# Optimization experiments

Hardware: AMD Instinct MI355X
Metric: run time of the kernel (lower is better)

## Reference

```python
import jax, jax.numpy as jnp
import numpy as np

B, C, H, W = 4, 64, 64, 64  # x shape; mask is (B,1,8H,8W)


def _conv(x, w, pad=0):
    return jax.lax.conv_general_dilated(
        x, w, (1, 1), [(pad, pad), (pad, pad)],
        dimension_numbers=('NCHW', 'OIHW', 'NCHW'))


def _inorm(x, eps=1e-5):  # InstanceNorm2d, affine=False, biased var (torch default)
    mu = x.mean(axis=(2, 3), keepdims=True)
    var = x.var(axis=(2, 3), keepdims=True)
    return (x - mu) * jax.lax.rsqrt(var + eps)


def _forward(x, mask, kconv_w1, kconv_w2, fs_w1, fs_w2, fs_b2, fs_fuse_w):
    b, c, h, w = x.shape
    n = h * w
    # MaxPool2d(8,8) then binarize
    m = jax.lax.reduce_window(mask, -jnp.inf, jax.lax.max,
                              (1, 1, 8, 8), (1, 1, 8, 8), 'VALID')
    m = (m > 0).astype(x.dtype)
    back = 1.0 - m
    # ResidualBlock K_conv (shared for K and Q paths in original code)
    y = jax.nn.relu(_inorm(_conv(x, kconv_w1, pad=1)))
    y = _inorm(_conv(y, kconv_w2, pad=1))
    kx = jax.nn.relu(y + x)
    # L2-normalized K/Q over channel dim
    K = (kx * back).reshape(b, c, n)
    K = K / (jnp.linalg.norm(K, axis=1, keepdims=True) + 1e-8)
    Q = (kx * m).reshape(b, c, n)
    Q = Q / (jnp.linalg.norm(Q, axis=1, keepdims=True) + 1e-8)
    V = (x * back).reshape(b, c, n)
    # cosine-similarity score map, temperature 20
    score = jnp.einsum('bcq,bck->bqk', Q, K) * 20.0  # (b, n_q, n_k)
    qm = m.reshape(b, 1, n)      # query mask (foreground)
    km = back.reshape(b, 1, n)   # key mask (background)
    NEG = -1000000.0
    validx = score + (1.0 - km) * NEG + (1.0 - qm.transpose(0, 2, 1)) * NEG
    att = jax.nn.softmax(validx, axis=-1) * (qm.transpose(0, 2, 1) * km)
    # att_fore[b,c,q] = sum_k V[b,c,k] * att[b,q,k]
    att_fore = jnp.einsum('bck,bqk->bcq', V, att).reshape(b, c, h, w)
    # Fusion_score
    feat1 = _conv(jnp.concatenate([x * m, att_fore * m], axis=1), fs_w1)
    s = jax.nn.sigmoid(_conv(feat1, fs_w2) + fs_b2[None, :, None, None])
    fused = _conv(jnp.concatenate([x * m, att_fore * m * (1.0 - s)], axis=1), fs_fuse_w)
    fs_out = fused * m + x * (1.0 - m)
    out = fs_out * m + x * (1.0 - m)
    # visualization attention mask
    visatt = att.sum(axis=1).reshape(b, 1, h, w)
    attmask = jnp.repeat(jnp.repeat(visatt, 8, axis=2), 8, axis=3)  # nearest upsample x8
    attmask = attmask / attmask.max()
    return out, attmask


def setup_inputs() -> dict:
    key = jax.random.key(0)
    ks = jax.random.split(key, 8)

    def wgt(k, shape, fan_in):
        return jax.random.normal(k, shape, jnp.float32) / np.sqrt(fan_in)

    x = jax.random.normal(ks[0], (B, C, H, W), jnp.float32)
    # sparse foreground mask so maxpool(8x8)>0 yields a mixed fg/bg mask
    mask = (jax.random.uniform(ks[1], (B, 1, H * 8, W * 8)) < 0.01).astype(jnp.float32)
    return dict(
        x=x, mask=mask,
        kconv_w1=wgt(ks[2], (C, C, 3, 3), C * 9),
        kconv_w2=wgt(ks[3], (C, C, 3, 3), C * 9),
        fs_w1=wgt(ks[4], (C, 2 * C, 1, 1), 2 * C),
        fs_w2=wgt(ks[5], (C, C, 1, 1), C),
        fs_b2=jnp.zeros((C,), jnp.float32),
        fs_fuse_w=wgt(ks[6], (C, 2 * C, 1, 1), 2 * C),
    )


def reference(x, mask, kconv_w1, kconv_w2, fs_w1, fs_w2, fs_b2, fs_fuse_w):
    return _forward(x, mask, kconv_w1, kconv_w2, fs_w1, fs_w2, fs_b2, fs_fuse_w)
```

## Files before the change

kernel.cpp:

```cpp
#include <hip/hip_runtime.h>
#include <hip/hip_bf16.h>

typedef __hip_bfloat16 bf16;
typedef __attribute__((ext_vector_type(8))) short short8;
typedef __attribute__((ext_vector_type(4))) float f32x4;
typedef __attribute__((ext_vector_type(16))) float f32x16;

#define BB 4
#define CC 64
#define NN 4096
#define MH 512
#define MW 512
#define LS 72

#define WB_AFC  ((size_t)0)
#define WB_DEN  ((size_t)4194304)
#define WB_VIS  ((size_t)4259840)
#define WB_QIX  ((size_t)4325376)
#define WB_KIX  ((size_t)4390912)
#define WB_MFL  ((size_t)4456448)
#define WB_CNT  ((size_t)4472832)
#define WB_STAT ((size_t)4472896)
#define WB_WT1  ((size_t)4476992)
#define WB_WT2  ((size_t)4550720)
#define WB_WFB  ((size_t)4624448)

__device__ __forceinline__ float b2f(bf16 v) { return __bfloat162float(v); }
__device__ __forceinline__ float us2f(unsigned short u) { return __uint_as_float(((unsigned)u) << 16); }
__device__ __forceinline__ unsigned short f2bu(float f) {
  bf16 h = __float2bfloat16(f);
  return *(unsigned short*)&h;
}

__global__ __launch_bounds__(256) void k_maxpool(const float* __restrict__ mask,
                                                 unsigned char* __restrict__ mfl,
                                                 float* __restrict__ vis,
                                                 float* __restrict__ gstat,
                                                 unsigned int* __restrict__ vmaxb) {
  int g = blockIdx.x * 256 + threadIdx.x;
  int o = g >> 2, sub = g & 3;
  int b = o >> 12, p = o & 4095;
  int py = p >> 6, px = p & 63;
  const float* mb = mask + (size_t)b * MH * MW + (py * 8 + sub * 2) * MW + px * 8;
  float mx = 0.f;
  #pragma unroll
  for (int dy = 0; dy < 2; ++dy) {
    const float4* r4 = (const float4*)(mb + dy * MW);
    float4 a = r4[0], c = r4[1];
    mx = fmaxf(mx, fmaxf(fmaxf(a.x, a.y), fmaxf(a.z, a.w)));
    mx = fmaxf(mx, fmaxf(fmaxf(c.x, c.y), fmaxf(c.z, c.w)));
  }
  mx = fmaxf(mx, __shfl_xor(mx, 1));
  mx = fmaxf(mx, __shfl_xor(mx, 2));
  if (sub == 0) {
    mfl[o] = (mx > 0.f) ? 1 : 0;
    vis[o] = 0.f;
  }
  if (g < 1024) gstat[g] = 0.f;
  if (g == 0) vmaxb[0] = 0u;
}

__global__ __launch_bounds__(64) void k_compact(const unsigned char* __restrict__ mfl,
                                                int* __restrict__ qidx, int* __restrict__ kidx,
                                                int* __restrict__ nq, int* __restrict__ nk) {
  int b = blockIdx.x, lane = threadIdx.x;
  int qb = 0, kb = 0;
  for (int it = 0; it < 64; ++it) {
    int p = it * 64 + lane;
    bool f = mfl[b * NN + p] != 0;
    unsigned long long bal = __ballot(f);
    int before = __popcll(bal & ((1ULL << lane) - 1ULL));
    if (f)  qidx[b * NN + qb + before] = p;
    if (!f) kidx[b * NN + kb + (lane - before)] = p;
    int cnt = __popcll(bal);
    qb += cnt; kb += 64 - cnt;
  }
  if (lane == 0) { nq[b] = qb; nk[b] = kb; }
}

__global__ __launch_bounds__(256) void k_xT(const float* __restrict__ x,
                                            unsigned short* __restrict__ xt) {
  int b = blockIdx.x >> 6, p0 = (blockIdx.x & 63) * 64;
  __shared__ float lx[64][65];
  int t = threadIdx.x;
  const float* xb = x + (size_t)b * CC * NN + p0;
  for (int idx = t; idx < 4096; idx += 256) {
    int c = idx >> 6, j = idx & 63;
    lx[j][c] = xb[c * NN + j];
  }
  __syncthreads();
  unsigned short* xo = xt + ((size_t)b * NN + p0) * 64;
  for (int idx = t; idx < 2048; idx += 256) {
    int j = idx >> 5, c2 = (idx & 31) * 2;
    ushort2 w2;
    w2.x = f2bu(lx[j][c2]);
    w2.y = f2bu(lx[j][c2 + 1]);
    *(ushort2*)&xo[j * 64 + c2] = w2;
  }
}

__global__ __launch_bounds__(256) void k_wprep(const float* __restrict__ w1,
                                               const float* __restrict__ w2,
                                               const float* __restrict__ fw1,
                                               const float* __restrict__ fw2,
                                               const float* __restrict__ fwf,
                                               unsigned short* __restrict__ wT1,
                                               unsigned short* __restrict__ wT2,
                                               unsigned short* __restrict__ wfb) {
  int i = blockIdx.x * 256 + threadIdx.x;
  if (i < 36864) {
    int tap = i >> 12;
    int rem = i & 4095;
    int co = rem >> 6, ci = rem & 63;
    int src = (co * 64 + ci) * 9 + tap;
    wT1[i] = f2bu(w1[src]);
    wT2[i] = f2bu(w2[src]);
  } else if (i < 57344) {
    int j = i - 36864;
    if (j < 8192)       wfb[j] = f2bu(fw1[j]);
    else if (j < 12288) wfb[j] = f2bu(fw2[j - 8192]);
    else                wfb[j] = f2bu(fwf[j - 12288]);
  }
}

template <bool NORM_IN>
__global__ __launch_bounds__(256) void k_convm(const unsigned short* __restrict__ src,
                                               const unsigned short* __restrict__ wT,
                                               const float* __restrict__ insum,
                                               const float* __restrict__ insq,
                                               unsigned short* __restrict__ dst,
                                               float* __restrict__ gsum,
                                               float* __restrict__ gsq) {
  int b = blockIdx.y;
  int r = blockIdx.x;
  __shared__ unsigned short bx[198 * LS];
  __shared__ float nmean[64], ninv[64];
  int t = threadIdx.x;
  if (NORM_IN) {
    if (t < 64) {
      float m = insum[b * 64 + t] * (1.f / NN);
      float v = fmaxf(insq[b * 64 + t] * (1.f / NN) - m * m, 0.f);
      nmean[t] = m; ninv[t] = rsqrtf(v + 1e-5f);
    }
    __syncthreads();
  }
  const unsigned short* sb = src + (size_t)b * NN * 64;
  for (int idx = t; idx < 198 * 8; idx += 256) {
    int row = idx >> 3, c8 = (idx & 7) * 8;
    int dy = row / 66;
    int cx = row - dy * 66 - 1;
    int rr = r + dy - 1;
    uint4 v = make_uint4(0u, 0u, 0u, 0u);
    if ((unsigned)rr < 64u && (unsigned)cx < 64u) {
      v = *(const uint4*)(sb + ((size_t)(rr * 64 + cx)) * 64 + c8);
      if (NORM_IN) {
        unsigned short* e = (unsigned short*)&v;
        #pragma unroll
        for (int j = 0; j < 8; ++j)
          e[j] = f2bu(fmaxf((us2f(e[j]) - nmean[c8 + j]) * ninv[c8 + j], 0.f));
      }
    }
    *(uint4*)&bx[row * LS + c8] = v;
  }
  __syncthreads();
  int lane = t & 63;
  int quad = lane >> 4, col = lane & 15;
  int qw = (t >> 6) * 16;
  f32x4 acc[4] = {{0.f,0.f,0.f,0.f},{0.f,0.f,0.f,0.f},{0.f,0.f,0.f,0.f},{0.f,0.f,0.f,0.f}};
  #pragma unroll
  for (int tap = 0; tap < 9; ++tap) {
    int dy = tap / 3, dx = tap - dy * 3 - 1;
    const unsigned short* wrow = wT + ((size_t)tap * 64 + qw + col) * 64;
    short8 a0 = *(const short8*)(wrow + quad * 8);
    short8 a1 = *(const short8*)(wrow + 32 + quad * 8);
    int rbase = dy * 66 + dx + 1;
    #pragma unroll
    for (int nt = 0; nt < 4; ++nt) {
      int row = rbase + nt * 16 + col;
      short8 b0 = *(const short8*)&bx[row * LS + quad * 8];
      short8 b1 = *(const short8*)&bx[row * LS + 32 + quad * 8];
      acc[nt] = __builtin_amdgcn_mfma_f32_16x16x32_bf16(a0, b0, acc[nt], 0, 0, 0);
      acc[nt] = __builtin_amdgcn_mfma_f32_16x16x32_bf16(a1, b1, acc[nt], 0, 0, 0);
    }
  }
  #pragma unroll
  for (int rr = 0; rr < 4; ++rr) {
    float s1 = acc[0][rr] + acc[1][rr] + acc[2][rr] + acc[3][rr];
    float s2 = acc[0][rr]*acc[0][rr] + acc[1][rr]*acc[1][rr]
             + acc[2][rr]*acc[2][rr] + acc[3][rr]*acc[3][rr];
    s1 += __shfl_xor(s1, 1); s2 += __shfl_xor(s2, 1);
    s1 += __shfl_xor(s1, 2); s2 += __shfl_xor(s2, 2);
    s1 += __shfl_xor(s1, 4); s2 += __shfl_xor(s2, 4);
    s1 += __shfl_xor(s1, 8); s2 += __shfl_xor(s2, 8);
    if (col == 0) {
      int co = qw + quad * 4 + rr;
      atomicAdd(&gsum[b * 64 + co], s1);
      atomicAdd(&gsq[b * 64 + co], s2);
    }
  }
  __syncthreads();
  #pragma unroll
  for (int nt = 0; nt < 4; ++nt)
    #pragma unroll
    for (int rr = 0; rr < 4; ++rr)
      bx[(nt * 16 + col) * LS + qw + quad * 4 + rr] = f2bu(acc[nt][rr]);
  __syncthreads();
  unsigned short* db = dst + ((size_t)b * NN + r * 64) * 64;
  for (int idx = t; idx < 512; idx += 256) {
    int px = idx >> 3, c8 = (idx & 7) * 8;
    *(uint4*)(db + (size_t)px * 64 + c8) = *(const uint4*)&bx[px * LS + c8];
  }
}

__global__ __launch_bounds__(256) void k_knorm(unsigned short* __restrict__ kxt,
                                               const unsigned short* __restrict__ xt,
                                               const float* __restrict__ gsum,
                                               const float* __restrict__ gsq,
                                               float* __restrict__ afc,
                                               float* __restrict__ den) {
  int b = blockIdx.x >> 6;
  int p0 = (blockIdx.x & 63) * 64;
  __shared__ float m2[64], i2[64];
  int t = threadIdx.x;
  if (t < 64) {
    float m = gsum[b * 64 + t] * (1.f / NN);
    float v = fmaxf(gsq[b * 64 + t] * (1.f / NN) - m * m, 0.f);
    m2[t] = m; i2[t] = rsqrtf(v + 1e-5f);
  }
  size_t gid = (size_t)blockIdx.x * 256 + t;
  float4 z4 = make_float4(0.f, 0.f, 0.f, 0.f);
  float4* az = (float4*)afc;
  #pragma unroll
  for (int j = 0; j < 4; ++j) az[gid + (size_t)j * 65536] = z4;
  if (gid < 16384) den[gid] = 0.f;
  __syncthreads();
  int px = t >> 2, c0 = (t & 3) * 16;
  size_t base = ((size_t)b * NN + p0 + px) * 64 + c0;
  unsigned short kv[16], xv[16];
  *(uint4*)&kv[0] = *(const uint4*)(kxt + base);
  *(uint4*)&kv[8] = *(const uint4*)(kxt + base + 8);
  *(uint4*)&xv[0] = *(const uint4*)(xt + base);
  *(uint4*)&xv[8] = *(const uint4*)(xt + base + 8);
  float v[16]; float ss = 0.f;
  #pragma unroll
  for (int j = 0; j < 16; ++j) {
    float f = fmaxf((us2f(kv[j]) - m2[c0 + j]) * i2[c0 + j] + us2f(xv[j]), 0.f);
    v[j] = f; ss += f * f;
  }
  ss += __shfl_xor(ss, 1);
  ss += __shfl_xor(ss, 2);
  float inv = 1.f / (sqrtf(ss) + 1e-8f);
  #pragma unroll
  for (int j = 0; j < 16; ++j) kv[j] = f2bu(v[j] * inv);
  *(uint4*)(kxt + base) = *(const uint4*)&kv[0];
  *(uint4*)(kxt + base + 8) = *(const uint4*)&kv[8];
}

__global__ __launch_bounds__(256) void k_att1(const unsigned short* __restrict__ khat,
                                              const unsigned short* __restrict__ xt,
                                              const int* __restrict__ qidx, const int* __restrict__ kidx,
                                              const int* __restrict__ nqv, const int* __restrict__ nkv,
                                              float* __restrict__ afc, float* __restrict__ den) {
  int b = blockIdx.y;
  int nqb = nqv[b], nkb = nkv[b];
  int q0 = (blockIdx.x >> 3) * 64;
  int part = blockIdx.x & 7;
  if (q0 >= nqb) return;
  int kbeg = (part * nkb) >> 3;
  int kend = ((part + 1) * nkb) >> 3;
  __shared__ unsigned short lk [64 * LS];
  __shared__ unsigned short lvT[64 * LS];
  __shared__ unsigned short le [64 * LS];
  int t = threadIdx.x;
  int wave = t >> 6, lane = t & 63;
  int l31 = lane & 31, lhi = lane >> 5;
  int qh = wave >> 1, kh = wave & 1;
  const int* qix = qidx + b * NN;
  const int* kix = kidx + b * NN;
  const unsigned short* khb = khat + (size_t)b * NN * 64;
  const unsigned short* xtb = xt + (size_t)b * NN * 64;
  int qq_a = q0 + qh * 32 + l31;
  int qp_a = (qq_a < nqb) ? qix[qq_a] : qix[0];
  short8 aq[4];
  #pragma unroll
  for (int ks = 0; ks < 4; ++ks)
    aq[ks] = *(const short8*)(khb + (size_t)qp_a * 64 + ks * 16 + lhi * 8);
  f32x16 pv, dsum;
  #pragma unroll
  for (int i = 0; i < 16; ++i) { pv[i] = 0.f; dsum[i] = 0.f; }
  int kp2 = t >> 3, vc8 = (t & 7) * 8, vcc = (t & 7);
  for (int j0 = kbeg; j0 < kend; j0 += 64) {
    __syncthreads();
    for (int idx = t; idx < 512; idx += 256) {
      int k = idx >> 3, c8 = (idx & 7) * 8;
      uint4 v = make_uint4(0u, 0u, 0u, 0u);
      if (j0 + k < kend) v = *(const uint4*)(khb + (size_t)kix[j0 + k] * 64 + c8);
      *(uint4*)&lk[k * LS + c8] = v;
    }
    {
      uint4 v0 = make_uint4(0u, 0u, 0u, 0u);
      uint4 v1 = make_uint4(0u, 0u, 0u, 0u);
      int ka = j0 + 2 * kp2, kb2 = ka + 1;
      if (ka  < kend) v0 = *(const uint4*)(xtb + (size_t)kix[ka]  * 64 + vc8);
      if (kb2 < kend) v1 = *(const uint4*)(xtb + (size_t)kix[kb2] * 64 + vc8);
      const unsigned short* e0 = (const unsigned short*)&v0;
      const unsigned short* e1 = (const unsigned short*)&v1;
      int pbase = kp2 & 3, prun = kp2 >> 2;
      int pp = pbase + ((prun ^ vcc) << 2);
      #pragma unroll
      for (int jj = 0; jj < 8; ++jj) {
        int c = vc8 + jj;
        unsigned int w2 = (unsigned)e0[jj] | ((unsigned)e1[jj] << 16);
        *(unsigned int*)&lvT[c * LS + pp * 2] = w2;
      }
    }
    __syncthreads();
    f32x16 s;
    #pragma unroll
    for (int i = 0; i < 16; ++i) s[i] = 0.f;
    #pragma unroll
    for (int ks = 0; ks < 4; ++ks) {
      short8 bk = *(const short8*)&lk[(kh * 32 + l31) * LS + ks * 16 + lhi * 8];
      s = __builtin_amdgcn_mfma_f32_32x32x16_bf16(aq[ks], bk, s, 0, 0, 0);
    }
    bool kval = (j0 + kh * 32 + l31) < kend;
    #pragma unroll
    for (int reg = 0; reg < 16; ++reg) {
      float e = kval ? __expf(20.f * s[reg]) : 0.f;
      dsum[reg] += e;
      int row = (reg & 3) + 8 * (reg >> 2) + 4 * lhi;
      le[(qh * 32 + row) * LS + kh * 32 + l31] = f2bu(e);
    }
    __syncthreads();
    int c = kh * 32 + l31;
    int c37 = (c >> 3) & 7;
    #pragma unroll
    for (int ks = 0; ks < 4; ++ks) {
      short8 a  = *(const short8*)&le[(qh * 32 + l31) * LS + ks * 16 + lhi * 8];
      int run = ks * 2 + lhi;
      short8 bv = *(const short8*)&lvT[c * LS + ((run ^ c37) << 3)];
      pv = __builtin_amdgcn_mfma_f32_32x32x16_bf16(a, bv, pv, 0, 0, 0);
    }
  }
  #pragma unroll
  for (int reg = 0; reg < 16; ++reg) {
    float v = dsum[reg];
    v += __shfl_xor(v, 1); v += __shfl_xor(v, 2); v += __shfl_xor(v, 4);
    v += __shfl_xor(v, 8); v += __shfl_xor(v, 16);
    int row = (reg & 3) + 8 * (reg >> 2) + 4 * lhi;
    int qq = q0 + qh * 32 + row;
    if (l31 == 0 && qq < nqb) atomicAdd(&den[b * NN + qq], v);
  }
  #pragma unroll
  for (int reg = 0; reg < 16; ++reg) {
    int row = (reg & 3) + 8 * (reg >> 2) + 4 * lhi;
    int qq = q0 + qh * 32 + row;
    if (qq < nqb) atomicAdd(&afc[((size_t)b * NN + qq) * 64 + kh * 32 + l31], pv[reg]);
  }
}

__global__ __launch_bounds__(256) void k_att2(const unsigned short* __restrict__ khat,
                                              const int* __restrict__ qidx, const int* __restrict__ kidx,
                                              const int* __restrict__ nqv, const int* __restrict__ nkv,
                                              const float* __restrict__ den, float* __restrict__ vis) {
  int b = blockIdx.y;
  int nqb = nqv[b], nkb = nkv[b];
  int k0 = (blockIdx.x >> 3) * 64;
  int part = blockIdx.x & 7;
  if (k0 >= nkb) return;
  int qbeg = (part * nqb) >> 3;
  int qend = ((part + 1) * nqb) >> 3;
  __shared__ unsigned short lq[64 * LS];
  __shared__ float w[64];
  int t = threadIdx.x;
  int wave = t >> 6, lane = t & 63;
  int l31 = lane & 31, lhi = lane >> 5;
  int kh = wave >> 1, qh = wave & 1;
  const int* qix = qidx + b * NN;
  const int* kix = kidx + b * NN;
  const unsigned short* khb = khat + (size_t)b * NN * 64;
  int kk_a = k0 + kh * 32 + l31;
  int kp_a = (kk_a < nkb) ? kix[kk_a] : kix[0];
  short8 ak[4];
  #pragma unroll
  for (int ks = 0; ks < 4; ++ks)
    ak[ks] = *(const short8*)(khb + (size_t)kp_a * 64 + ks * 16 + lhi * 8);
  f32x16 vacc;
  #pragma unroll
  for (int i = 0; i < 16; ++i) vacc[i] = 0.f;
  for (int i0 = qbeg; i0 < qend; i0 += 64) {
    __syncthreads();
    for (int idx = t; idx < 512; idx += 256) {
      int q = idx >> 3, c8 = (idx & 7) * 8;
      uint4 v = make_uint4(0u, 0u, 0u, 0u);
      if (i0 + q < qend) v = *(const uint4*)(khb + (size_t)qix[i0 + q] * 64 + c8);
      *(uint4*)&lq[q * LS + c8] = v;
    }
    if (t < 64) {
      int qq = i0 + t;
      float d = (qq < qend) ? den[b * NN + qq] : 0.f;
      w[t] = (d > 0.f) ? 1.f / d : 0.f;
    }
    __syncthreads();
    f32x16 s;
    #pragma unroll
    for (int i = 0; i < 16; ++i) s[i] = 0.f;
    #pragma unroll
    for (int ks = 0; ks < 4; ++ks) {
      short8 bq = *(const short8*)&lq[(qh * 32 + l31) * LS + ks * 16 + lhi * 8];
      s = __builtin_amdgcn_mfma_f32_32x32x16_bf16(ak[ks], bq, s, 0, 0, 0);
    }
    float wq = w[qh * 32 + l31];
    #pragma unroll
    for (int reg = 0; reg < 16; ++reg) vacc[reg] += __expf(20.f * s[reg]) * wq;
  }
  #pragma unroll
  for (int reg = 0; reg < 16; ++reg) {
    float v = vacc[reg];
    v += __shfl_xor(v, 1); v += __shfl_xor(v, 2); v += __shfl_xor(v, 4);
    v += __shfl_xor(v, 8); v += __shfl_xor(v, 16);
    int row = (reg & 3) + 8 * (reg >> 2) + 4 * lhi;
    int kk = k0 + kh * 32 + row;
    if (l31 == 0 && kk < nkb) atomicAdd(&vis[b * NN + kix[kk]], v);
  }
}

__global__ __launch_bounds__(256) void k_copy(const uint4* __restrict__ src, uint4* __restrict__ dst, int n) {
  int i = blockIdx.x * 256 + threadIdx.x;
  if (i < n) dst[i] = src[i];
}

#define FS 136
__global__ __launch_bounds__(256) void k_fusionm(const unsigned short* __restrict__ xt,
                                                 const float* __restrict__ afc,
                                                 const float* __restrict__ den,
                                                 const int* __restrict__ qidx, const int* __restrict__ nqv,
                                                 const unsigned short* __restrict__ wall,
                                                 const float* __restrict__ b2,
                                                 float* __restrict__ outp) {
  int b = blockIdx.y;
  int nqb = nqv[b];
  int q0 = blockIdx.x * 64;
  if (q0 >= nqb) return;
  __shared__ unsigned short pxa[64 * FS];
  __shared__ unsigned short f1s[64 * LS];
  __shared__ int qpl[64];
  int t = threadIdx.x;
  int lane = t & 63;
  int quad = lane >> 4, col = lane & 15;
  int cb = (t >> 6) * 16;
  const int* qix = qidx + b * NN;
  const unsigned short* xtb = xt + (size_t)b * NN * 64;
  const unsigned short* w1b = wall;
  const unsigned short* w2b = wall + 8192;
  const unsigned short* wfb = wall + 12288;
  short8 a1[4], a2[2], af[4];
  #pragma unroll
  for (int kt = 0; kt < 4; ++kt) {
    a1[kt] = *(const short8*)&w1b[(cb + col) * 128 + kt * 32 + quad * 8];
    af[kt] = *(const short8*)&wfb[(cb + col) * 128 + kt * 32 + quad * 8];
  }
  #pragma unroll
  for (int kt = 0; kt < 2; ++kt)
    a2[kt] = *(const short8*)&w2b[(cb + col) * 64 + kt * 32 + quad * 8];
  float b2v[4];
  #pragma unroll
  for (int r = 0; r < 4; ++r) b2v[r] = b2[cb + quad * 4 + r];
  if (t < 64) qpl[t] = (q0 + t < nqb) ? qix[q0 + t] : -1;
  for (int idx = t; idx < 512; idx += 256) {
    int q = idx >> 3, c8 = (idx & 7) * 8;
    int qq = q0 + q;
    uint4 pv = make_uint4(0u, 0u, 0u, 0u);
    unsigned short pa8[8] = {0, 0, 0, 0, 0, 0, 0, 0};
    if (qq < nqb) {
      int qp = qix[qq];
      pv = *(const uint4*)(xtb + (size_t)qp * 64 + c8);
      float d = den[b * NN + qq];
      float invd = (d > 0.f) ? 1.f / d : 0.f;
      const float* ap = afc + ((size_t)b * NN + qq) * 64 + c8;
      #pragma unroll
      for (int j = 0; j < 8; ++j) pa8[j] = f2bu(ap[j] * invd);
    }
    *(uint4*)&pxa[q * FS + c8] = pv;
    *(uint4*)&pxa[q * FS + 64 + c8] = *(const uint4*)&pa8[0];
  }
  __syncthreads();
  #pragma unroll
  for (int qt = 0; qt < 4; ++qt) {
    f32x4 acc = {0.f, 0.f, 0.f, 0.f};
    #pragma unroll
    for (int kt = 0; kt < 4; ++kt) {
      short8 bfrag = *(const short8*)&pxa[(qt * 16 + col) * FS + kt * 32 + quad * 8];
      acc = __builtin_amdgcn_mfma_f32_16x16x32_bf16(a1[kt], bfrag, acc, 0, 0, 0);
    }
    #pragma unroll
    for (int r = 0; r < 4; ++r)
      f1s[(qt * 16 + col) * LS + cb + quad * 4 + r] = f2bu(acc[r]);
  }
  __syncthreads();
  #pragma unroll
  for (int qt = 0; qt < 4; ++qt) {
    f32x4 acc = {0.f, 0.f, 0.f, 0.f};
    #pragma unroll
    for (int kt = 0; kt < 2; ++kt) {
      short8 bfrag = *(const short8*)&f1s[(qt * 16 + col) * LS + kt * 32 + quad * 8];
      acc = __builtin_amdgcn_mfma_f32_16x16x32_bf16(a2[kt], bfrag, acc, 0, 0, 0);
    }
    #pragma unroll
    for (int r = 0; r < 4; ++r) {
      float sg = 1.f / (1.f + __expf(-(acc[r] + b2v[r])));
      int addr = (qt * 16 + col) * FS + 64 + cb + quad * 4 + r;
      pxa[addr] = f2bu(us2f(pxa[addr]) * (1.f - sg));
    }
  }
  __syncthreads();
  #pragma unroll
  for (int qt = 0; qt < 4; ++qt) {
    f32x4 acc = {0.f, 0.f, 0.f, 0.f};
    #pragma unroll
    for (int kt = 0; kt < 4; ++kt) {
      short8 bfrag = *(const short8*)&pxa[(qt * 16 + col) * FS + kt * 32 + quad * 8];
      acc = __builtin_amdgcn_mfma_f32_16x16x32_bf16(af[kt], bfrag, acc, 0, 0, 0);
    }
    int qp = qpl[qt * 16 + col];
    if (qp >= 0) {
      #pragma unroll
      for (int r = 0; r < 4; ++r)
        outp[((size_t)b * CC + cb + quad * 4 + r) * NN + qp] = acc[r];
    }
  }
}

__global__ __launch_bounds__(256) void k_vmax(const float* __restrict__ vis, unsigned int* __restrict__ vmaxb) {
  int i = blockIdx.x * 256 + threadIdx.x;
  float v = vis[i];
  #pragma unroll
  for (int off = 32; off > 0; off >>= 1) v = fmaxf(v, __shfl_down(v, off));
  if ((threadIdx.x & 63) == 0) atomicMax(vmaxb, __float_as_uint(v));
}

__global__ __launch_bounds__(256) void k_upsample(const float* __restrict__ vis,
                                                  const unsigned int* __restrict__ vmaxb,
                                                  float* __restrict__ out2) {
  int i = blockIdx.x * 256 + threadIdx.x;
  int b = i >> 18;
  int rem = i & 262143;
  int y = rem >> 9, x = rem & 511;
  float vm = __uint_as_float(vmaxb[0]);
  if (!(vm > 0.f)) vm = 1.f;
  out2[i] = vis[b * NN + (y >> 3) * 64 + (x >> 3)] / vm;
}

extern "C" void kernel_launch(void* const* d_in, const int* in_sizes, int n_in,
                              void* d_out, int out_size, void* d_ws, size_t ws_size,
                              hipStream_t stream) {
  const float* x    = (const float*)d_in[0];
  const float* mask = (const float*)d_in[1];
  const float* w1   = (const float*)d_in[2];
  const float* w2c  = (const float*)d_in[3];
  const float* fsw1 = (const float*)d_in[4];
  const float* fsw2 = (const float*)d_in[5];
  const float* fsb2 = (const float*)d_in[6];
  const float* fswf = (const float*)d_in[7];
  float* out = (float*)d_out;
  char* wsb = (char*)d_ws;

  float* afc = (float*)(wsb + WB_AFC);
  float* den = (float*)(wsb + WB_DEN);
  float* vis = (float*)(wsb + WB_VIS);
  int* qidx  = (int*)(wsb + WB_QIX);
  int* kidx  = (int*)(wsb + WB_KIX);
  unsigned char* mfl = (unsigned char*)(wsb + WB_MFL);
  int* nq = (int*)(wsb + WB_CNT);
  int* nk = nq + 4;
  unsigned int* vmaxb = (unsigned int*)(nq + 8);
  float* gstat = (float*)(wsb + WB_STAT);
  float* gsum1 = gstat;
  float* gsq1  = gstat + 256;
  float* gsum2 = gstat + 512;
  float* gsq2  = gstat + 768;
  unsigned short* wT1 = (unsigned short*)(wsb + WB_WT1);
  unsigned short* wT2 = (unsigned short*)(wsb + WB_WT2);
  unsigned short* wall = (unsigned short*)(wsb + WB_WFB);
  unsigned short* y1t = (unsigned short*)(wsb + WB_AFC);

  unsigned short* kxt = (unsigned short*)out;
  unsigned short* khat = kxt;
  unsigned short* xt = (unsigned short*)(out + 1048576);

  k_maxpool<<<256, 256, 0, stream>>>(mask, mfl, vis, gstat, vmaxb);
  k_compact<<<4, 64, 0, stream>>>(mfl, qidx, kidx, nq, nk);
  k_xT<<<256, 256, 0, stream>>>(x, xt);
  k_wprep<<<224, 256, 0, stream>>>(w1, w2c, fsw1, fsw2, fswf, wT1, wT2, wall);
  k_convm<false><<<dim3(64, BB), 256, 0, stream>>>(xt, wT1, nullptr, nullptr, y1t, gsum1, gsq1);
  k_convm<true><<<dim3(64, BB), 256, 0, stream>>>(y1t, wT2, gsum1, gsq1, kxt, gsum2, gsq2);
  k_knorm<<<256, 256, 0, stream>>>(kxt, xt, gsum2, gsq2, afc, den);
  k_att1<<<dim3(512, BB), 256, 0, stream>>>(khat, xt, qidx, kidx, nq, nk, afc, den);
  k_att2<<<dim3(512, BB), 256, 0, stream>>>(khat, qidx, kidx, nq, nk, den, vis);
  k_copy<<<1024, 256, 0, stream>>>((const uint4*)x, (uint4*)out, 262144);
  k_fusionm<<<dim3(64, BB), 256, 0, stream>>>(xt, afc, den, qidx, nq, wall, fsb2, out);
  k_vmax<<<64, 256, 0, stream>>>(vis, vmaxb);
  k_upsample<<<4096, 256, 0, stream>>>(vis, vmaxb, out + 1048576);
}
```

Baseline: 194.3 us.

## Store exp scores in att1 and replace att2 recompute with streaming vis reduction

```diff
diff --git a/kernel.cpp b/kernel.cpp
--- a/kernel.cpp
+++ b/kernel.cpp
@@ -24,6 +24,10 @@
 #define WB_WT1  ((size_t)4476992)
 #define WB_WT2  ((size_t)4550720)
 #define WB_WFB  ((size_t)4624448)
+#define WB_XT   ((size_t)8388608)
+#define WB_KXT  ((size_t)10485760)
+#define WB_E    ((size_t)16777216)
+#define EB_ELEM ((size_t)8388608)
 
 __device__ __forceinline__ float b2f(bf16 v) { return __bfloat162float(v); }
 __device__ __forceinline__ float us2f(unsigned short u) { return __uint_as_float(((unsigned)u) << 16); }
@@ -32,42 +36,96 @@
   return *(unsigned short*)&h;
 }
 
-__global__ __launch_bounds__(256) void k_maxpool(const float* __restrict__ mask,
-                                                 unsigned char* __restrict__ mfl,
-                                                 float* __restrict__ vis,
-                                                 float* __restrict__ gstat,
-                                                 unsigned int* __restrict__ vmaxb) {
-  int g = blockIdx.x * 256 + threadIdx.x;
-  int o = g >> 2, sub = g & 3;
-  int b = o >> 12, p = o & 4095;
-  int py = p >> 6, px = p & 63;
-  const float* mb = mask + (size_t)b * MH * MW + (py * 8 + sub * 2) * MW + px * 8;
-  float mx = 0.f;
-  #pragma unroll
-  for (int dy = 0; dy < 2; ++dy) {
-    const float4* r4 = (const float4*)(mb + dy * MW);
-    float4 a = r4[0], c = r4[1];
-    mx = fmaxf(mx, fmaxf(fmaxf(a.x, a.y), fmaxf(a.z, a.w)));
-    mx = fmaxf(mx, fmaxf(fmaxf(c.x, c.y), fmaxf(c.z, c.w)));
-  }
-  mx = fmaxf(mx, __shfl_xor(mx, 1));
-  mx = fmaxf(mx, __shfl_xor(mx, 2));
-  if (sub == 0) {
-    mfl[o] = (mx > 0.f) ? 1 : 0;
-    vis[o] = 0.f;
-  }
-  if (g < 1024) gstat[g] = 0.f;
-  if (g == 0) vmaxb[0] = 0u;
-}
-
-__global__ __launch_bounds__(64) void k_compact(const unsigned char* __restrict__ mfl,
-                                                int* __restrict__ qidx, int* __restrict__ kidx,
-                                                int* __restrict__ nq, int* __restrict__ nk) {
-  int b = blockIdx.x, lane = threadIdx.x;
+__global__ __launch_bounds__(256) void k_pre(const float* __restrict__ x,
+                                             const float* __restrict__ mask,
+                                             const float* __restrict__ w1,
+                                             const float* __restrict__ w2,
+                                             const float* __restrict__ fw1,
+                                             const float* __restrict__ fw2,
+                                             const float* __restrict__ fwf,
+                                             float* __restrict__ outp,
+                                             unsigned short* __restrict__ xt,
+                                             unsigned char* __restrict__ mfl,
+                                             float* __restrict__ vis,
+                                             float* __restrict__ gstat,
+                                             unsigned int* __restrict__ vmaxb,
+                                             unsigned short* __restrict__ wT1,
+                                             unsigned short* __restrict__ wT2,
+                                             unsigned short* __restrict__ wfb) {
+  __shared__ float lx[64][65];
+  int t = threadIdx.x;
+  if (blockIdx.x < 256) {
+    int b = blockIdx.x >> 6, p0 = (blockIdx.x & 63) * 64;
+    const float* xb = x + (size_t)b * CC * NN + p0;
+    float* ob = outp + (size_t)b * CC * NN + p0;
+    for (int idx = t; idx < 4096; idx += 256) {
+      int c = idx >> 6, j = idx & 63;
+      float v = xb[c * NN + j];
+      lx[j][c] = v;
+      ob[c * NN + j] = v;
+    }
+    __syncthreads();
+    unsigned short* xo = xt + ((size_t)b * NN + p0) * 64;
+    for (int idx = t; idx < 2048; idx += 256) {
+      int j = idx >> 5, c2 = (idx & 31) * 2;
+      ushort2 w2v;
+      w2v.x = f2bu(lx[j][c2]);
+      w2v.y = f2bu(lx[j][c2 + 1]);
+      *(ushort2*)&xo[j * 64 + c2] = w2v;
+    }
+  } else {
+    int g = (blockIdx.x - 256) * 256 + t;
+    int o = g >> 2, sub = g & 3;
+    int b = o >> 12, p = o & 4095;
+    int py = p >> 6, px = p & 63;
+    const float* mb = mask + (size_t)b * MH * MW + (py * 8 + sub * 2) * MW + px * 8;
+    float mx = 0.f;
+    #pragma unroll
+    for (int dy = 0; dy < 2; ++dy) {
+      const float4* r4 = (const float4*)(mb + dy * MW);
+      float4 a = r4[0], c = r4[1];
+      mx = fmaxf(mx, fmaxf(fmaxf(a.x, a.y), fmaxf(a.z, a.w)));
+      mx = fmaxf(mx, fmaxf(fmaxf(c.x, c.y), fmaxf(c.z, c.w)));
+    }
+    mx = fmaxf(mx, __shfl_xor(mx, 1));
+    mx = fmaxf(mx, __shfl_xor(mx, 2));
+    if (sub == 0) {
+      mfl[o] = (mx > 0.f) ? 1 : 0;
+      vis[o] = 0.f;
+    }
+    if (g < 1024) gstat[g] = 0.f;
+    if (g == 0) vmaxb[0] = 0u;
+    if (g < 36864) {
+      int tap = g >> 12;
+      int rem = g & 4095;
+      int co = rem >> 6, ci = rem & 63;
+      int src = (co * 64 + ci) * 9 + tap;
+      wT1[g] = f2bu(w1[src]);
+      wT2[g] = f2bu(w2[src]);
+    } else if (g < 57344) {
+      int j2 = g - 36864;
+      if (j2 < 8192)       wfb[j2] = f2bu(fw1[j2]);
+      else if (j2 < 12288) wfb[j2] = f2bu(fw2[j2 - 8192]);
+      else                 wfb[j2] = f2bu(fwf[j2 - 12288]);
+    }
+  }
+}
+
+__global__ __launch_bounds__(256) void k_compact(const unsigned char* __restrict__ mfl,
+                                                 int* __restrict__ qidx, int* __restrict__ kidx,
+                                                 int* __restrict__ nq, int* __restrict__ nk) {
+  int b = blockIdx.x;
+  __shared__ unsigned char lm[4096];
+  int t = threadIdx.x;
+  *(uint4*)&lm[t * 16] = *(const uint4*)&mfl[b * NN + t * 16];
+  __syncthreads();
+  if (t >= 64) return;
+  int lane = t;
   int qb = 0, kb = 0;
+  #pragma unroll
   for (int it = 0; it < 64; ++it) {
     int p = it * 64 + lane;
-    bool f = mfl[b * NN + p] != 0;
+    bool f = lm[p] != 0;
     unsigned long long bal = __ballot(f);
     int before = __popcll(bal & ((1ULL << lane) - 1ULL));
     if (f)  qidx[b * NN + qb + before] = p;
@@ -76,51 +134,6 @@
     qb += cnt; kb += 64 - cnt;
   }
   if (lane == 0) { nq[b] = qb; nk[b] = kb; }
-}
-
-__global__ __launch_bounds__(256) void k_xT(const float* __restrict__ x,
-                                            unsigned short* __restrict__ xt) {
-  int b = blockIdx.x >> 6, p0 = (blockIdx.x & 63) * 64;
-  __shared__ float lx[64][65];
-  int t = threadIdx.x;
-  const float* xb = x + (size_t)b * CC * NN + p0;
-  for (int idx = t; idx < 4096; idx += 256) {
-    int c = idx >> 6, j = idx & 63;
-    lx[j][c] = xb[c * NN + j];
-  }
-  __syncthreads();
-  unsigned short* xo = xt + ((size_t)b * NN + p0) * 64;
-  for (int idx = t; idx < 2048; idx += 256) {
-    int j = idx >> 5, c2 = (idx & 31) * 2;
-    ushort2 w2;
-    w2.x = f2bu(lx[j][c2]);
-    w2.y = f2bu(lx[j][c2 + 1]);
-    *(ushort2*)&xo[j * 64 + c2] = w2;
-  }
-}
-
-__global__ __launch_bounds__(256) void k_wprep(const float* __restrict__ w1,
-                                               const float* __restrict__ w2,
-                                               const float* __restrict__ fw1,
-                                               const float* __restrict__ fw2,
-                                               const float* __restrict__ fwf,
-                                               unsigned short* __restrict__ wT1,
-                                               unsigned short* __restrict__ wT2,
-                                               unsigned short* __restrict__ wfb) {
-  int i = blockIdx.x * 256 + threadIdx.x;
-  if (i < 36864) {
-    int tap = i >> 12;
-    int rem = i & 4095;
-    int co = rem >> 6, ci = rem & 63;
-    int src = (co * 64 + ci) * 9 + tap;
-    wT1[i] = f2bu(w1[src]);
-    wT2[i] = f2bu(w2[src]);
-  } else if (i < 57344) {
-    int j = i - 36864;
-    if (j < 8192)       wfb[j] = f2bu(fw1[j]);
-    else if (j < 12288) wfb[j] = f2bu(fw2[j - 8192]);
-    else                wfb[j] = f2bu(fwf[j - 12288]);
-  }
 }
 
 template <bool NORM_IN>
@@ -260,7 +273,8 @@
                                               const unsigned short* __restrict__ xt,
                                               const int* __restrict__ qidx, const int* __restrict__ kidx,
                                               const int* __restrict__ nqv, const int* __restrict__ nkv,
-                                              float* __restrict__ afc, float* __restrict__ den) {
+                                              float* __restrict__ afc, float* __restrict__ den,
+                                              unsigned short* __restrict__ eg) {
   int b = blockIdx.y;
   int nqb = nqv[b], nkb = nkv[b];
   int q0 = (blockIdx.x >> 3) * 64;
@@ -268,6 +282,7 @@
   if (q0 >= nqb) return;
   int kbeg = (part * nkb) >> 3;
   int kend = ((part + 1) * nkb) >> 3;
+  int NKP = (nkb + 63) & ~63;
   __shared__ unsigned short lk [64 * LS];
   __shared__ unsigned short lvT[64 * LS];
   __shared__ unsigned short le [64 * LS];
@@ -279,6 +294,7 @@
   const int* kix = kidx + b * NN;
   const unsigned short* khb = khat + (size_t)b * NN * 64;
   const unsigned short* xtb = xt + (size_t)b * NN * 64;
+  unsigned short* egb = eg + (size_t)b * EB_ELEM;
   int qq_a = q0 + qh * 32 + l31;
   int qp_a = (qq_a < nqb) ? qix[qq_a] : qix[0];
   short8 aq[4];
@@ -324,12 +340,16 @@
       s = __builtin_amdgcn_mfma_f32_32x32x16_bf16(aq[ks], bk, s, 0, 0, 0);
     }
     bool kval = (j0 + kh * 32 + l31) < kend;
+    unsigned short* egc = egb + (size_t)(j0 + kh * 32 + l31);
     #pragma unroll
     for (int reg = 0; reg < 16; ++reg) {
       float e = kval ? __expf(20.f * s[reg]) : 0.f;
       dsum[reg] += e;
       int row = (reg & 3) + 8 * (reg >> 2) + 4 * lhi;
-      le[(qh * 32 + row) * LS + kh * 32 + l31] = f2bu(e);
+      unsigned short eh = f2bu(e);
+      le[(qh * 32 + row) * LS + kh * 32 + l31] = eh;
+      int qq = q0 + qh * 32 + row;
+      if (kval && qq < nqb) egc[(size_t)qq * NKP] = eh;
     }
     __syncthreads();
     int c = kh * 32 + l31;
@@ -359,75 +379,44 @@
   }
 }
 
-__global__ __launch_bounds__(256) void k_att2(const unsigned short* __restrict__ khat,
-                                              const int* __restrict__ qidx, const int* __restrict__ kidx,
-                                              const int* __restrict__ nqv, const int* __restrict__ nkv,
-                                              const float* __restrict__ den, float* __restrict__ vis) {
-  int b = blockIdx.y;
+__global__ __launch_bounds__(256) void k_vis(const unsigned short* __restrict__ eg,
+                                             const float* __restrict__ den,
+                                             const int* __restrict__ kidx,
+                                             const int* __restrict__ nqv, const int* __restrict__ nkv,
+                                             float* __restrict__ vis) {
+  int b = blockIdx.z;
   int nqb = nqv[b], nkb = nkv[b];
-  int k0 = (blockIdx.x >> 3) * 64;
-  int part = blockIdx.x & 7;
+  int k0 = blockIdx.x * 256;
   if (k0 >= nkb) return;
-  int qbeg = (part * nqb) >> 3;
-  int qend = ((part + 1) * nqb) >> 3;
-  __shared__ unsigned short lq[64 * LS];
-  __shared__ float w[64];
-  int t = threadIdx.x;
-  int wave = t >> 6, lane = t & 63;
-  int l31 = lane & 31, lhi = lane >> 5;
-  int kh = wave >> 1, qh = wave & 1;
-  const int* qix = qidx + b * NN;
-  const int* kix = kidx + b * NN;
-  const unsigned short* khb = khat + (size_t)b * NN * 64;
-  int kk_a = k0 + kh * 32 + l31;
-  int kp_a = (kk_a < nkb) ? kix[kk_a] : kix[0];
-  short8 ak[4];
-  #pragma unroll
-  for (int ks = 0; ks < 4; ++ks)
-    ak[ks] = *(const short8*)(khb + (size_t)kp_a * 64 + ks * 16 + lhi * 8);
-  f32x16 vacc;
-  #pragma unroll
-  for (int i = 0; i < 16; ++i) vacc[i] = 0.f;
-  for (int i0 = qbeg; i0 < qend; i0 += 64) {
-    __syncthreads();
-    for (int idx = t; idx < 512; idx += 256) {
-      int q = idx >> 3, c8 = (idx & 7) * 8;
-      uint4 v = make_uint4(0u, 0u, 0u, 0u);
-      if (i0 + q < qend) v = *(const uint4*)(khb + (size_t)qix[i0 + q] * 64 + c8);
-      *(uint4*)&lq[q * LS + c8] = v;
-    }
-    if (t < 64) {
-      int qq = i0 + t;
-      float d = (qq < qend) ? den[b * NN + qq] : 0.f;
-      w[t] = (d > 0.f) ? 1.f / d : 0.f;
-    }
-    __syncthreads();
-    f32x16 s;
-    #pragma unroll
-    for (int i = 0; i < 16; ++i) s[i] = 0.f;
-    #pragma unroll
-    for (int ks = 0; ks < 4; ++ks) {
-      short8 bq = *(const short8*)&lq[(qh * 32 + l31) * LS + ks * 16 + lhi * 8];
-      s = __builtin_amdgcn_mfma_f32_32x32x16_bf16(ak[ks], bq, s, 0, 0, 0);
-    }
-    float wq = w[qh * 32 + l31];
-    #pragma unroll
-    for (int reg = 0; reg < 16; ++reg) vacc[reg] += __expf(20.f * s[reg]) * wq;
-  }
-  #pragma unroll
-  for (int reg = 0; reg < 16; ++reg) {
-    float v = vacc[reg];
-    v += __shfl_xor(v, 1); v += __shfl_xor(v, 2); v += __shfl_xor(v, 4);
-    v += __shfl_xor(v, 8); v += __shfl_xor(v, 16);
-    int row = (reg & 3) + 8 * (reg >> 2) + 4 * lhi;
-    int kk = k0 + kh * 32 + row;
-    if (l31 == 0 && kk < nkb) atomicAdd(&vis[b * NN + kix[kk]], v);
-  }
-}
-
-__global__ __launch_bounds__(256) void k_copy(const uint4* __restrict__ src, uint4* __restrict__ dst, int n) {
-  int i = blockIdx.x * 256 + threadIdx.x;
-  if (i < n) dst[i] = src[i];
+  int NKP = (nkb + 63) & ~63;
+  int qpart = blockIdx.y;
+  int qbeg = (qpart * nqb) >> 3;
+  int qend = ((qpart + 1) * nqb) >> 3;
+  __shared__ float wd[256];
+  int t = threadIdx.x;
+  int k = k0 + t;
+  const unsigned short* eb = eg + (size_t)b * EB_ELEM;
+  float acc = 0.f;
+  for (int qc = qbeg; qc < qend; qc += 256) {
+    __syncthreads();
+    int qq = qc + t;
+    float d = (qq < qend) ? den[b * NN + qq] : 0.f;
+    wd[t] = (d > 0.f) ? 1.f / d : 0.f;
+    __syncthreads();
+    int lim = min(256, qend - qc);
+    if (k < nkb) {
+      const unsigned short* ep = eb + (size_t)qc * NKP + k;
+      int j = 0;
+      for (; j + 8 <= lim; j += 8) {
+        #pragma unroll
+        for (int u = 0; u < 8; ++u)
+          acc += us2f(ep[(size_t)(j + u) * NKP]) * wd[j + u];
+      }
+      for (; j < lim; ++j)
+        acc += us2f(ep[(size_t)j * NKP]) * wd[j];
+    }
+  }
+  if (k < nkb) atomicAdd(&vis[b * NN + kidx[b * NN + k]], acc);
 }
 
 #define FS 136
@@ -583,21 +572,19 @@
   unsigned short* wT2 = (unsigned short*)(wsb + WB_WT2);
   unsigned short* wall = (unsigned short*)(wsb + WB_WFB);
   unsigned short* y1t = (unsigned short*)(wsb + WB_AFC);
-
-  unsigned short* kxt = (unsigned short*)out;
+  unsigned short* xt  = (unsigned short*)(wsb + WB_XT);
+  unsigned short* kxt = (unsigned short*)(wsb + WB_KXT);
   unsigned short* khat = kxt;
-  unsigned short* xt = (unsigned short*)(out + 1048576);
-
-  k_maxpool<<<256, 256, 0, stream>>>(mask, mfl, vis, gstat, vmaxb);
-  k_compact<<<4, 64, 0, stream>>>(mfl, qidx, kidx, nq, nk);
-  k_xT<<<256, 256, 0, stream>>>(x, xt);
-  k_wprep<<<224, 256, 0, stream>>>(w1, w2c, fsw1, fsw2, fswf, wT1, wT2, wall);
+  unsigned short* eg  = (unsigned short*)(wsb + WB_E);
+
+  k_pre<<<512, 256, 0, stream>>>(x, mask, w1, w2c, fsw1, fsw2, fswf,
+                                 out, xt, mfl, vis, gstat, vmaxb, wT1, wT2, wall);
+  k_compact<<<4, 256, 0, stream>>>(mfl, qidx, kidx, nq, nk);
   k_convm<false><<<dim3(64, BB), 256, 0, stream>>>(xt, wT1, nullptr, nullptr, y1t, gsum1, gsq1);
   k_convm<true><<<dim3(64, BB), 256, 0, stream>>>(y1t, wT2, gsum1, gsq1, kxt, gsum2, gsq2);
   k_knorm<<<256, 256, 0, stream>>>(kxt, xt, gsum2, gsq2, afc, den);
-  k_att1<<<dim3(512, BB), 256, 0, stream>>>(khat, xt, qidx, kidx, nq, nk, afc, den);
-  k_att2<<<dim3(512, BB), 256, 0, stream>>>(khat, qidx, kidx, nq, nk, den, vis);
-  k_copy<<<1024, 256, 0, stream>>>((const uint4*)x, (uint4*)out, 262144);
+  k_att1<<<dim3(512, BB), 256, 0, stream>>>(khat, xt, qidx, kidx, nq, nk, afc, den, eg);
+  k_vis<<<dim3(16, 8, BB), 256, 0, stream>>>(eg, den, kidx, nq, nk, vis);
   k_fusionm<<<dim3(64, BB), 256, 0, stream>>>(xt, afc, den, qidx, nq, wall, fsb2, out);
   k_vmax<<<64, 256, 0, stream>>>(vis, vmaxb);
   k_upsample<<<4096, 256, 0, stream>>>(vis, vmaxb, out + 1048576);
```

Measured after the change: 191.2 us. Within noise of the previous version (-1.6%).
